# Kernel optimization log

Hardware: AMD Instinct MI355X
Metric: run time of the kernel (lower is better)

The kernel has to match this reference:

```python
import jax, jax.numpy as jnp
import numpy as np

B, T, D = 64, 128, 1024
E = 2048      # embedding_dim of state encoder
CD = 256      # VQ code_dim
NC = 1024     # num_codes
BETA = 0.25   # commitment cost


def setup_inputs() -> dict:
    key = jax.random.key(0)
    ks = jax.random.split(key, 5)
    states = jax.random.normal(ks[0], (B, T, D), dtype=jnp.float32)
    next_states = jax.random.normal(ks[1], (B, T, D), dtype=jnp.float32)
    # VarianceScaling(scale=2.0, fan_in) init
    W_s = jax.random.normal(ks[2], (D, E), dtype=jnp.float32) * np.sqrt(2.0 / D)
    b_s = jnp.zeros((E,), dtype=jnp.float32)
    W_p = jax.random.normal(ks[3], (2 * E, CD), dtype=jnp.float32) * np.sqrt(2.0 / (2 * E))
    b_p = jnp.zeros((CD,), dtype=jnp.float32)
    codebook = jax.random.normal(ks[4], (NC, CD), dtype=jnp.float32)
    return {"states": states, "next_states": next_states, "W_s": W_s,
            "b_s": b_s, "W_p": W_p, "b_p": b_p, "codebook": codebook}


def reference(states, next_states, W_s, b_s, W_p, b_p, codebook):
    # dual state encoder (shared weights)
    se = states @ W_s + b_s            # (B,T,E)
    ne = next_states @ W_s + b_s       # (B,T,E)
    policy_input = jax.nn.gelu(jnp.concatenate([se, ne], axis=-1))  # (B,T,2E)
    latent = policy_input @ W_p + b_p  # (B,T,CD)

    # --- VectorQuantizerEMA forward ---
    flat = latent.reshape(-1, CD)      # (N, CD), N = B*T
    # squared euclidean distances to codebook rows
    dists = (jnp.sum(flat * flat, axis=1, keepdims=True)
             - 2.0 * flat @ codebook.T
             + jnp.sum(codebook * codebook, axis=1))  # (N, NC)
    idx = jnp.argmin(dists, axis=1)                    # (N,)
    encodings = jax.nn.one_hot(idx, NC, dtype=latent.dtype)  # (N, NC)
    quantize = codebook[idx].reshape(latent.shape)     # (B,T,CD)

    e_latent_loss = jnp.mean(jnp.square(jax.lax.stop_gradient(quantize) - latent))
    loss = BETA * e_latent_loss
    # straight-through estimator
    quantize_st = latent + jax.lax.stop_gradient(quantize - latent)

    avg_probs = jnp.mean(encodings, axis=0)
    perplexity = jnp.exp(-jnp.sum(avg_probs * jnp.log(avg_probs + 1e-10)))

    encodings = encodings.reshape(B, T, NC)
    encoding_indices = idx.reshape(B, T)
    return quantize_st, loss, perplexity, encodings, encoding_indices
```

## Files before the change

kernel.cpp:

```cpp
#include <hip/hip_runtime.h>

#define NROW  8192
#define D_    1024
#define E_    2048
#define P2E_  4096
#define CD_   256
#define NC_   1024
#define BETA_ 0.25f
#define SPLITK 8

typedef __attribute__((ext_vector_type(8))) short short8;
typedef __attribute__((ext_vector_type(4))) float f32x4;

__device__ __forceinline__ ushort f2bf(float x) {
    union { float f; unsigned u; } v; v.f = x;
    unsigned r = (v.u + 0x7fffu + ((v.u >> 16) & 1u)) >> 16;
    return (ushort)r;
}
__device__ __forceinline__ float bf2f(ushort h) {
    union { unsigned u; float f; } v; v.u = ((unsigned)h) << 16;
    return v.f;
}
__device__ __forceinline__ void split2(float x, ushort& h, ushort& l) {
    h = f2bf(x);
    l = f2bf(x - bf2f(h));
}
__device__ __forceinline__ float gelu_tanh(float x) {
    float x3 = x * x * x;
    return 0.5f * x * (1.0f + tanhf(0.7978845608028654f * (x + 0.044715f * x3)));
}

#define GLD16(gp, lp) __builtin_amdgcn_global_load_lds( \
    (const __attribute__((address_space(1))) void*)(gp), \
    (__attribute__((address_space(3))) void*)(lp), 16, 0, 0)

template<int EPI>
__global__ __launch_bounds__(256)
void gemm_bf16x3(const ushort* __restrict__ Ah, const ushort* __restrict__ Al,
                 const ushort* __restrict__ Bh, const ushort* __restrict__ Bl,
                 int K, int ksteps,
                 const float* __restrict__ bias,
                 float* __restrict__ outF,
                 ushort* __restrict__ oPh, ushort* __restrict__ oPl,
                 const float* __restrict__ cn,
                 float* __restrict__ candv, int* __restrict__ candi)
{
    __shared__ alignas(16) ushort sAh[4096], sAl[4096], sBh[4096], sBl[4096];
    const int t = threadIdx.x;
    const int l = t & 63;
    const int w = t >> 6;
    const int wr = w >> 1, wc = w & 1;

    const int nxy = gridDim.x * gridDim.y;
    const int id  = blockIdx.y * gridDim.x + blockIdx.x;
    const int swz = (id & 7) * (nxy >> 3) + (id >> 3);
    const int bx  = swz % gridDim.x;
    const int by  = swz / gridDim.x;

    const int bm = by * 128;
    const int bn = bx * 128;
    const int kstart = (EPI == 1) ? (int)blockIdx.z * (ksteps * 32) : 0;

    const int srow = t >> 2;
    const int scol = ((t & 3) ^ ((t >> 3) & 3)) * 8;
    const ushort* gAh = Ah + (size_t)(bm + srow) * K + kstart + scol;
    const ushort* gAl = Al + (size_t)(bm + srow) * K + kstart + scol;
    const ushort* gBh = Bh + (size_t)(bn + srow) * K + kstart + scol;
    const ushort* gBl = Bl + (size_t)(bn + srow) * K + kstart + scol;
    const size_t rstep = (size_t)64 * K;
    const int lo0 = t * 8, lo1 = t * 8 + 2048;

    f32x4 acc[4][4];
#pragma unroll
    for (int i = 0; i < 4; i++)
#pragma unroll
        for (int j = 0; j < 4; j++) acc[i][j] = (f32x4)0.0f;

    const int rsw = ((l >> 4) ^ (((l & 15) >> 1) & 3)) * 8;
    const int ar = (wr * 64 + (l & 15)) * 32 + rsw;
    const int br = (wc * 64 + (l & 15)) * 32 + rsw;

#define STAGE8() do { \
        GLD16(gAh, &sAh[lo0]); GLD16(gAh + rstep, &sAh[lo1]); \
        GLD16(gAl, &sAl[lo0]); GLD16(gAl + rstep, &sAl[lo1]); \
        GLD16(gBh, &sBh[lo0]); GLD16(gBh + rstep, &sBh[lo1]); \
        GLD16(gBl, &sBl[lo0]); GLD16(gBl + rstep, &sBl[lo1]); \
    } while (0)

    STAGE8();
    __syncthreads();

    for (int s = 0; s < ksteps; ++s) {
        short8 fah[4], fal[4], fbh[4], fbl[4];
#pragma unroll
        for (int i = 0; i < 4; i++) {
            fah[i] = *(const short8*)&sAh[ar + i * 16 * 32];
            fal[i] = *(const short8*)&sAl[ar + i * 16 * 32];
            fbh[i] = *(const short8*)&sBh[br + i * 16 * 32];
            fbl[i] = *(const short8*)&sBl[br + i * 16 * 32];
        }
        __syncthreads();

        if (s + 1 < ksteps) {
            gAh += 32; gAl += 32; gBh += 32; gBl += 32;
            STAGE8();
        }

        __builtin_amdgcn_s_setprio(1);
#pragma unroll
        for (int i = 0; i < 4; i++)
#pragma unroll
            for (int j = 0; j < 4; j++) {
                acc[i][j] = __builtin_amdgcn_mfma_f32_16x16x32_bf16(fah[i], fbh[j], acc[i][j], 0, 0, 0);
                acc[i][j] = __builtin_amdgcn_mfma_f32_16x16x32_bf16(fah[i], fbl[j], acc[i][j], 0, 0, 0);
                acc[i][j] = __builtin_amdgcn_mfma_f32_16x16x32_bf16(fal[i], fbh[j], acc[i][j], 0, 0, 0);
            }
        __builtin_amdgcn_s_setprio(0);
        __syncthreads();
    }
#undef STAGE8

    if constexpr (EPI == 2) {
        float (*redv)[2] = (float(*)[2])sAh;
        int   (*redi)[2] = (int(*)[2])sAl;
        float cnv[4];
#pragma unroll
        for (int j = 0; j < 4; j++) cnv[j] = cn[bn + wc * 64 + j * 16 + (l & 15)];
#pragma unroll
        for (int i = 0; i < 4; i++) {
            const int grow = bm + wr * 64 + i * 16 + (l >> 4) * 4;
#pragma unroll
            for (int r = 0; r < 4; r++) {
                float bv = INFINITY; int bi = 0;
#pragma unroll
                for (int j = 0; j < 4; j++) {
                    float d = cnv[j] - 2.0f * acc[i][j][r];
                    int c = bn + wc * 64 + j * 16 + (l & 15);
                    if (d < bv) { bv = d; bi = c; }
                }
#pragma unroll
                for (int m = 1; m < 16; m <<= 1) {
                    float ov = __shfl_xor(bv, m, 64);
                    int   oi = __shfl_xor(bi, m, 64);
                    if (ov < bv || (ov == bv && oi < bi)) { bv = ov; bi = oi; }
                }
                int rl = wr * 64 + i * 16 + (l >> 4) * 4 + r;
                if ((l & 15) == 0) { redv[rl][wc] = bv; redi[rl][wc] = bi; }
#pragma unroll
                for (int j = 0; j < 4; j++)
                    outF[(size_t)(grow + r) * NC_ + bn + wc * 64 + j * 16 + (l & 15)] = 0.0f;
            }
        }
        __syncthreads();
        if (t < 128) {
            float v0 = redv[t][0], v1 = redv[t][1];
            int   i0 = redi[t][0], i1 = redi[t][1];
            bool take1 = (v1 < v0) || (v1 == v0 && i1 < i0);
            candv[(size_t)(bm + t) * 8 + bx] = take1 ? v1 : v0;
            candi[(size_t)(bm + t) * 8 + bx] = take1 ? i1 : i0;
        }
        return;
    }

#pragma unroll
    for (int i = 0; i < 4; i++) {
        const int grow = bm + wr * 64 + i * 16 + (l >> 4) * 4;
#pragma unroll
        for (int j = 0; j < 4; j++) {
            const int gcol = bn + wc * 64 + j * 16 + (l & 15);
            f32x4 a = acc[i][j];
            if constexpr (EPI == 0) {
                const float bb = bias[gcol];
#pragma unroll
                for (int r = 0; r < 4; r++) {
                    int m = grow + r;
                    float x = gelu_tanh(a[r] + bb);
                    ushort h, lo; split2(x, h, lo);
                    int pr = (m < NROW) ? m : m - NROW;
                    int pc = ((m < NROW) ? 0 : E_) + gcol;
                    oPh[(size_t)pr * P2E_ + pc] = h;
                    oPl[(size_t)pr * P2E_ + pc] = lo;
                }
            } else if constexpr (EPI == 1) {
                float* o = outF + ((size_t)NROW * blockIdx.z + grow) * CD_ + gcol;
#pragma unroll
                for (int r = 0; r < 4; r++) o[(size_t)r * CD_] = a[r];
            }
        }
    }
}

__global__ void split_k(const float* __restrict__ in, ushort* __restrict__ oh,
                        ushort* __restrict__ ol, int n4)
{
    int i = blockIdx.x * blockDim.x + threadIdx.x;
    int stride = gridDim.x * blockDim.x;
    for (; i < n4; i += stride) {
        float4 v = ((const float4*)in)[i];
        ushort4 h, lo;
        split2(v.x, h.x, lo.x); split2(v.y, h.y, lo.y);
        split2(v.z, h.z, lo.z); split2(v.w, h.w, lo.w);
        ((ushort4*)oh)[i] = h;
        ((ushort4*)ol)[i] = lo;
    }
}

__global__ __launch_bounds__(1024)
void tsplit_k(const float* __restrict__ in, ushort* __restrict__ oh,
              ushort* __restrict__ ol, int R, int C)
{
    __shared__ float tile[32][33];
    int c0 = blockIdx.x * 32, r0 = blockIdx.y * 32;
    int tx = threadIdx.x, ty = threadIdx.y;
    tile[ty][tx] = in[(size_t)(r0 + ty) * C + c0 + tx];
    __syncthreads();
    float x = tile[tx][ty];
    ushort h, lo; split2(x, h, lo);
    size_t o = (size_t)(c0 + ty) * R + r0 + tx;
    oh[o] = h; ol[o] = lo;
}

__global__ __launch_bounds__(256)
void combine_k(const float* __restrict__ part, const float* __restrict__ bias,
               float* __restrict__ latent, ushort* __restrict__ lh,
               ushort* __restrict__ ll)
{
    int row = blockIdx.x, t = threadIdx.x;
    float x = bias[t];
#pragma unroll
    for (int z = 0; z < SPLITK; z++) x += part[((size_t)z * NROW + row) * CD_ + t];
    latent[(size_t)row * CD_ + t] = x;
    ushort h, lo; split2(x, h, lo);
    lh[(size_t)row * CD_ + t] = h;
    ll[(size_t)row * CD_ + t] = lo;
}

__global__ __launch_bounds__(256) void row_norms(const float* __restrict__ X,
                                                 float* __restrict__ out)
{
    __shared__ float s[256];
    int n = blockIdx.x, t = threadIdx.x;
    float v = X[(size_t)n * 256 + t];
    s[t] = v * v;
    __syncthreads();
    for (int st = 128; st > 0; st >>= 1) {
        if (t < st) s[t] += s[t + st];
        __syncthreads();
    }
    if (t == 0) out[n] = s[0];
}

__global__ void zero_hist(int* hist) { hist[threadIdx.x] = 0; }

__global__ __launch_bounds__(256) void vq2_kernel(
    const float* __restrict__ latent, const float* __restrict__ cb,
    const float* __restrict__ candv, const int* __restrict__ candi,
    float* __restrict__ out_enc, float* __restrict__ out_q,
    float* __restrict__ out_idx, int* __restrict__ hist, float* __restrict__ lpart)
{
    __shared__ float sd[256];
    __shared__ int sbc;
    const int n = blockIdx.x, t = threadIdx.x;
    if (t == 0) {
        const float* cv = candv + (size_t)n * 8;
        const int*   ci = candi + (size_t)n * 8;
        float bv = cv[0]; int bi = ci[0];
#pragma unroll
        for (int k = 1; k < 8; k++) {
            float v = cv[k]; int x = ci[k];
            if (v < bv || (v == bv && x < bi)) { bv = v; bi = x; }
        }
        sbc = bi;
    }
    __syncthreads();
    const int bc = sbc;
    if (t == 0) out_enc[(size_t)n * NC_ + bc] = 1.0f;

    float lv = latent[(size_t)n * CD_ + t];
    float q  = cb[(size_t)bc * CD_ + t];
    out_q[(size_t)n * CD_ + t] = lv + (q - lv);
    float diff = q - lv;
    sd[t] = diff * diff;
    __syncthreads();
    for (int st = 128; st > 0; st >>= 1) {
        if (t < st) sd[t] += sd[t + st];
        __syncthreads();
    }
    if (t == 0) {
        lpart[n] = sd[0];
        atomicAdd(&hist[bc], 1);
        out_idx[n] = (float)bc;
    }
}

__global__ __launch_bounds__(1024) void finalize_kernel(
    const float* __restrict__ lpart, const int* __restrict__ hist,
    float* __restrict__ out_loss, float* __restrict__ out_perp)
{
    __shared__ float s[1024];
    int t = threadIdx.x;
    float x = 0.0f;
    for (int i = t; i < NROW; i += 1024) x += lpart[i];
    s[t] = x;
    __syncthreads();
    for (int st = 512; st > 0; st >>= 1) {
        if (t < st) s[t] += s[t + st];
        __syncthreads();
    }
    float total = s[0];
    __syncthreads();
    float p = (float)hist[t] * (1.0f / NROW);
    s[t] = p * logf(p + 1e-10f);
    __syncthreads();
    for (int st = 512; st > 0; st >>= 1) {
        if (t < st) s[t] += s[t + st];
        __syncthreads();
    }
    if (t == 0) {
        *out_loss = BETA_ * (total / (float)((size_t)NROW * CD_));
        *out_perp = expf(-s[0]);
    }
}

extern "C" void kernel_launch(void* const* d_in, const int* in_sizes, int n_in,
                              void* d_out, int out_size, void* d_ws, size_t ws_size,
                              hipStream_t stream)
{
    const float* states      = (const float*)d_in[0];
    const float* next_states = (const float*)d_in[1];
    const float* W_s         = (const float*)d_in[2];
    const float* b_s         = (const float*)d_in[3];
    const float* W_p         = (const float*)d_in[4];
    const float* b_p         = (const float*)d_in[5];
    const float* codebook    = (const float*)d_in[6];

    float* out      = (float*)d_out;
    float* out_q    = out;
    float* out_loss = out + (size_t)NROW * CD_;
    float* out_perp = out_loss + 1;
    float* out_enc  = out_perp + 1;
    float* out_idx  = out_enc + (size_t)NROW * NC_;

    char* ws = (char*)d_ws;
    size_t off = 0;
    auto alloc = [&](size_t bytes) { void* p = ws + off; off += (bytes + 255) & ~255ull; return p; };

    ushort* A1h  = (ushort*)alloc((size_t)2 * NROW * D_ * 2);
    ushort* A1l  = (ushort*)alloc((size_t)2 * NROW * D_ * 2);
    ushort* WsTh = (ushort*)alloc((size_t)E_ * D_ * 2);
    ushort* WsTl = (ushort*)alloc((size_t)E_ * D_ * 2);
    ushort* WpTh = (ushort*)alloc((size_t)CD_ * P2E_ * 2);
    ushort* WpTl = (ushort*)alloc((size_t)CD_ * P2E_ * 2);
    ushort* cbh  = (ushort*)alloc((size_t)NC_ * CD_ * 2);
    ushort* cbl  = (ushort*)alloc((size_t)NC_ * CD_ * 2);
    ushort* Ph   = (ushort*)alloc((size_t)NROW * P2E_ * 2);
    ushort* Pl   = (ushort*)alloc((size_t)NROW * P2E_ * 2);
    ushort* lath = (ushort*)alloc((size_t)NROW * CD_ * 2);
    ushort* latl = (ushort*)alloc((size_t)NROW * CD_ * 2);
    float*  cbn  = (float*)alloc(NC_ * 4);
    int*    hist = (int*)alloc(NC_ * 4);
    float*  lpart= (float*)alloc(NROW * 4);
    float*  candv= (float*)alloc((size_t)NROW * 8 * 4);
    int*    candi= (int*)alloc((size_t)NROW * 8 * 4);
    float* lat_part = (float*)A1h;
    float* latent   = (float*)WsTh;

    {
        int n4 = NROW * D_ / 4;
        split_k<<<2048, 256, 0, stream>>>(states, A1h, A1l, n4);
        split_k<<<2048, 256, 0, stream>>>(next_states, A1h + (size_t)NROW * D_,
                                          A1l + (size_t)NROW * D_, n4);
    }
    tsplit_k<<<dim3(E_ / 32, D_ / 32), dim3(32, 32), 0, stream>>>(W_s, WsTh, WsTl, D_, E_);
    tsplit_k<<<dim3(CD_ / 32, P2E_ / 32), dim3(32, 32), 0, stream>>>(W_p, WpTh, WpTl, P2E_, CD_);
    split_k<<<256, 256, 0, stream>>>(codebook, cbh, cbl, NC_ * CD_ / 4);
    row_norms<<<NC_, 256, 0, stream>>>(codebook, cbn);

    gemm_bf16x3<0><<<dim3(E_ / 128, 2 * NROW / 128), 256, 0, stream>>>(
        A1h, A1l, WsTh, WsTl, D_, D_ / 32, b_s, nullptr, Ph, Pl, nullptr, nullptr, nullptr);

    gemm_bf16x3<1><<<dim3(CD_ / 128, NROW / 128, SPLITK), 256, 0, stream>>>(
        Ph, Pl, WpTh, WpTl, P2E_, P2E_ / 32 / SPLITK, nullptr, lat_part, nullptr, nullptr,
        nullptr, nullptr, nullptr);

    combine_k<<<NROW, 256, 0, stream>>>(lat_part, b_p, latent, lath, latl);

    gemm_bf16x3<2><<<dim3(NC_ / 128, NROW / 128), 256, 0, stream>>>(
        lath, latl, cbh, cbl, CD_, CD_ / 32, nullptr, out_enc, nullptr, nullptr,
        cbn, candv, candi);

    zero_hist<<<1, NC_, 0, stream>>>(hist);
    vq2_kernel<<<NROW, 256, 0, stream>>>(latent, codebook, candv, candi,
                                         out_enc, out_q, out_idx, hist, lpart);
    finalize_kernel<<<1, 1024, 0, stream>>>(lpart, hist, out_loss, out_perp);
}
```

Before: 359.2 us.

## Enlarge GEMM M-tile to 256 rows and double-buffer the A tile

The bf16x3 GEMM tile grows from 128x128 to 256x128. Each wave now holds 8x4 accumulators, and the A operand is double-buffered in LDS, with A fragments loaded inside the MFMA loop instead of all being preloaded. Launch bounds now request 2 blocks per SM and all three GEMM grids are halved along M. The aim is more MFMA work per B tile load and fewer blocks, at the cost of higher register and LDS pressure (about 80KB LDS per block). B is still single-buffered, so a barrier per k-step remains.

After: 378.0 us. +5.2%, slower.

```diff
diff --git a/kernel.cpp b/kernel.cpp
--- a/kernel.cpp
+++ b/kernel.cpp
@@ -35,7 +35,7 @@
     (__attribute__((address_space(3))) void*)(lp), 16, 0, 0)
 
 template<int EPI>
-__global__ __launch_bounds__(256)
+__global__ __launch_bounds__(256, 2)
 void gemm_bf16x3(const ushort* __restrict__ Ah, const ushort* __restrict__ Al,
                  const ushort* __restrict__ Bh, const ushort* __restrict__ Bl,
                  int K, int ksteps,
@@ -45,7 +45,8 @@
                  const float* __restrict__ cn,
                  float* __restrict__ candv, int* __restrict__ candi)
 {
-    __shared__ alignas(16) ushort sAh[4096], sAl[4096], sBh[4096], sBl[4096];
+    __shared__ alignas(16) ushort sAh2[16384], sAl2[16384];
+    __shared__ alignas(16) ushort sBh[4096], sBl[4096];
     const int t = threadIdx.x;
     const int l = t & 63;
     const int w = t >> 6;
@@ -57,7 +58,7 @@
     const int bx  = swz % gridDim.x;
     const int by  = swz / gridDim.x;
 
-    const int bm = by * 128;
+    const int bm = by * 256;
     const int bn = bx * 128;
     const int kstart = (EPI == 1) ? (int)blockIdx.z * (ksteps * 32) : 0;
 
@@ -68,74 +69,87 @@
     const ushort* gBh = Bh + (size_t)(bn + srow) * K + kstart + scol;
     const ushort* gBl = Bl + (size_t)(bn + srow) * K + kstart + scol;
     const size_t rstep = (size_t)64 * K;
-    const int lo0 = t * 8, lo1 = t * 8 + 2048;
-
-    f32x4 acc[4][4];
-#pragma unroll
-    for (int i = 0; i < 4; i++)
+    const int d8 = t * 8;
+
+    f32x4 acc[8][4];
+#pragma unroll
+    for (int i = 0; i < 8; i++)
 #pragma unroll
         for (int j = 0; j < 4; j++) acc[i][j] = (f32x4)0.0f;
 
-    const int rsw = ((l >> 4) ^ (((l & 15) >> 1) & 3)) * 8;
-    const int ar = (wr * 64 + (l & 15)) * 32 + rsw;
-    const int br = (wc * 64 + (l & 15)) * 32 + rsw;
-
-#define STAGE8() do { \
-        GLD16(gAh, &sAh[lo0]); GLD16(gAh + rstep, &sAh[lo1]); \
-        GLD16(gAl, &sAl[lo0]); GLD16(gAl + rstep, &sAl[lo1]); \
-        GLD16(gBh, &sBh[lo0]); GLD16(gBh + rstep, &sBh[lo1]); \
-        GLD16(gBl, &sBl[lo0]); GLD16(gBl + rstep, &sBl[lo1]); \
-    } while (0)
-
-    STAGE8();
-    __syncthreads();
-
+    const int kq = l >> 4, lr = l & 15;
+    const int rsw = (kq ^ ((lr >> 1) & 3)) * 8;
+    const int ar0 = (wr * 128 + lr) * 32 + rsw;
+    const int br0 = (wc * 64 + lr) * 32 + rsw;
+
+#define STAGEA(buf, koff) do { \
+        _Pragma("unroll") \
+        for (int p = 0; p < 4; p++) { \
+            GLD16(gAh + (koff) + p * rstep, &sAh2[(buf) * 8192 + d8 + p * 2048]); \
+            GLD16(gAl + (koff) + p * rstep, &sAl2[(buf) * 8192 + d8 + p * 2048]); \
+        } } while (0)
+#define STAGEB(koff) do { \
+        _Pragma("unroll") \
+        for (int p = 0; p < 2; p++) { \
+            GLD16(gBh + (koff) + p * rstep, &sBh[d8 + p * 2048]); \
+            GLD16(gBl + (koff) + p * rstep, &sBl[d8 + p * 2048]); \
+        } } while (0)
+
+    STAGEA(0, 0);
+    STAGEB(0);
+    __syncthreads();
+
+    int cur = 0;
     for (int s = 0; s < ksteps; ++s) {
-        short8 fah[4], fal[4], fbh[4], fbl[4];
-#pragma unroll
-        for (int i = 0; i < 4; i++) {
-            fah[i] = *(const short8*)&sAh[ar + i * 16 * 32];
-            fal[i] = *(const short8*)&sAl[ar + i * 16 * 32];
-            fbh[i] = *(const short8*)&sBh[br + i * 16 * 32];
-            fbl[i] = *(const short8*)&sBl[br + i * 16 * 32];
+        short8 fbh[4], fbl[4];
+#pragma unroll
+        for (int j = 0; j < 4; j++) {
+            fbh[j] = *(const short8*)&sBh[br0 + j * 512];
+            fbl[j] = *(const short8*)&sBl[br0 + j * 512];
         }
         __syncthreads();
 
         if (s + 1 < ksteps) {
-            gAh += 32; gAl += 32; gBh += 32; gBl += 32;
-            STAGE8();
-        }
-
+            STAGEA(cur ^ 1, (s + 1) * 32);
+            STAGEB((s + 1) * 32);
+        }
+
+        const int ab = cur * 8192;
         __builtin_amdgcn_s_setprio(1);
 #pragma unroll
-        for (int i = 0; i < 4; i++)
+        for (int i = 0; i < 8; i++) {
+            short8 fah = *(const short8*)&sAh2[ab + ar0 + i * 512];
+            short8 fal = *(const short8*)&sAl2[ab + ar0 + i * 512];
 #pragma unroll
             for (int j = 0; j < 4; j++) {
-                acc[i][j] = __builtin_amdgcn_mfma_f32_16x16x32_bf16(fah[i], fbh[j], acc[i][j], 0, 0, 0);
-                acc[i][j] = __builtin_amdgcn_mfma_f32_16x16x32_bf16(fah[i], fbl[j], acc[i][j], 0, 0, 0);
-                acc[i][j] = __builtin_amdgcn_mfma_f32_16x16x32_bf16(fal[i], fbh[j], acc[i][j], 0, 0, 0);
+                acc[i][j] = __builtin_amdgcn_mfma_f32_16x16x32_bf16(fah, fbh[j], acc[i][j], 0, 0, 0);
+                acc[i][j] = __builtin_amdgcn_mfma_f32_16x16x32_bf16(fah, fbl[j], acc[i][j], 0, 0, 0);
+                acc[i][j] = __builtin_amdgcn_mfma_f32_16x16x32_bf16(fal, fbh[j], acc[i][j], 0, 0, 0);
             }
+        }
         __builtin_amdgcn_s_setprio(0);
         __syncthreads();
-    }
-#undef STAGE8
+        cur ^= 1;
+    }
+#undef STAGEA
+#undef STAGEB
 
     if constexpr (EPI == 2) {
-        float (*redv)[2] = (float(*)[2])sAh;
-        int   (*redi)[2] = (int(*)[2])sAl;
+        float (*redv)[2] = (float(*)[2])sBh;
+        int   (*redi)[2] = (int(*)[2])sBl;
         float cnv[4];
 #pragma unroll
-        for (int j = 0; j < 4; j++) cnv[j] = cn[bn + wc * 64 + j * 16 + (l & 15)];
-#pragma unroll
-        for (int i = 0; i < 4; i++) {
-            const int grow = bm + wr * 64 + i * 16 + (l >> 4) * 4;
+        for (int j = 0; j < 4; j++) cnv[j] = cn[bn + wc * 64 + j * 16 + lr];
+#pragma unroll
+        for (int i = 0; i < 8; i++) {
+            const int grow = bm + wr * 128 + i * 16 + kq * 4;
 #pragma unroll
             for (int r = 0; r < 4; r++) {
                 float bv = INFINITY; int bi = 0;
 #pragma unroll
                 for (int j = 0; j < 4; j++) {
                     float d = cnv[j] - 2.0f * acc[i][j][r];
-                    int c = bn + wc * 64 + j * 16 + (l & 15);
+                    int c = bn + wc * 64 + j * 16 + lr;
                     if (d < bv) { bv = d; bi = c; }
                 }
 #pragma unroll
@@ -144,15 +158,15 @@
                     int   oi = __shfl_xor(bi, m, 64);
                     if (ov < bv || (ov == bv && oi < bi)) { bv = ov; bi = oi; }
                 }
-                int rl = wr * 64 + i * 16 + (l >> 4) * 4 + r;
-                if ((l & 15) == 0) { redv[rl][wc] = bv; redi[rl][wc] = bi; }
+                int rl = wr * 128 + i * 16 + kq * 4 + r;
+                if (lr == 0) { redv[rl][wc] = bv; redi[rl][wc] = bi; }
 #pragma unroll
                 for (int j = 0; j < 4; j++)
-                    outF[(size_t)(grow + r) * NC_ + bn + wc * 64 + j * 16 + (l & 15)] = 0.0f;
+                    outF[(size_t)(grow + r) * NC_ + bn + wc * 64 + j * 16 + lr] = 0.0f;
             }
         }
         __syncthreads();
-        if (t < 128) {
+        {
             float v0 = redv[t][0], v1 = redv[t][1];
             int   i0 = redi[t][0], i1 = redi[t][1];
             bool take1 = (v1 < v0) || (v1 == v0 && i1 < i0);
@@ -163,11 +177,11 @@
     }
 
 #pragma unroll
-    for (int i = 0; i < 4; i++) {
-        const int grow = bm + wr * 64 + i * 16 + (l >> 4) * 4;
+    for (int i = 0; i < 8; i++) {
+        const int grow = bm + wr * 128 + i * 16 + kq * 4;
 #pragma unroll
         for (int j = 0; j < 4; j++) {
-            const int gcol = bn + wc * 64 + j * 16 + (l & 15);
+            const int gcol = bn + wc * 64 + j * 16 + lr;
             f32x4 a = acc[i][j];
             if constexpr (EPI == 0) {
                 const float bb = bias[gcol];
@@ -376,16 +390,16 @@
     split_k<<<256, 256, 0, stream>>>(codebook, cbh, cbl, NC_ * CD_ / 4);
     row_norms<<<NC_, 256, 0, stream>>>(codebook, cbn);
 
-    gemm_bf16x3<0><<<dim3(E_ / 128, 2 * NROW / 128), 256, 0, stream>>>(
+    gemm_bf16x3<0><<<dim3(E_ / 128, 2 * NROW / 256), 256, 0, stream>>>(
         A1h, A1l, WsTh, WsTl, D_, D_ / 32, b_s, nullptr, Ph, Pl, nullptr, nullptr, nullptr);
 
-    gemm_bf16x3<1><<<dim3(CD_ / 128, NROW / 128, SPLITK), 256, 0, stream>>>(
+    gemm_bf16x3<1><<<dim3(CD_ / 128, NROW / 256, SPLITK), 256, 0, stream>>>(
         Ph, Pl, WpTh, WpTl, P2E_, P2E_ / 32 / SPLITK, nullptr, lat_part, nullptr, nullptr,
         nullptr, nullptr, nullptr);
 
     combine_k<<<NROW, 256, 0, stream>>>(lat_part, b_p, latent, lath, latl);
 
-    gemm_bf16x3<2><<<dim3(NC_ / 128, NROW / 128), 256, 0, stream>>>(
+    gemm_bf16x3<2><<<dim3(NC_ / 128, NROW / 256), 256, 0, stream>>>(
         lath, latl, cbh, cbl, CD_, CD_ / 32, nullptr, out_enc, nullptr, nullptr,
         cbn, candv, candi);
 
```
